# Optimization experiments

Hardware: AMD Instinct MI355X
Metric: run time of the kernel (lower is better)

The kernel has to match this reference:

```python
import jax, jax.numpy as jnp
import numpy as np

NUM_TRUE = 8
NUM_NULL = 2
NUM_EXPERTS = NUM_TRUE + NUM_NULL
TOP_K = 2


def setup_inputs() -> dict:
    key = jax.random.key(0)
    k0, k1, k2 = jax.random.split(key, 3)
    B, S, D = 4, 2048, 1024
    inputs = jax.random.normal(k0, (B, S, D), dtype=jnp.float32)
    gate_w = jax.random.normal(k1, (NUM_EXPERTS, D), dtype=jnp.float32) * 0.02
    gate_b = jnp.zeros((NUM_EXPERTS,), dtype=jnp.float32)
    # expert_w stored as [E, D_in, D_out] so expert i computes x @ expert_w[i] + expert_b[i]
    expert_w = jax.random.normal(k2, (NUM_TRUE, D, D), dtype=jnp.float32) * 0.02
    expert_b = jnp.zeros((NUM_TRUE, D), dtype=jnp.float32)
    return {"inputs": inputs, "gate_w": gate_w, "gate_b": gate_b,
            "expert_w": expert_w, "expert_b": expert_b}


def reference(inputs, gate_w, gate_b, expert_w, expert_b):
    D = inputs.shape[-1]
    x = inputs.reshape(-1, D)                       # [T, D]
    gate_logits = x @ gate_w.T + gate_b             # [T, E]
    gate_probs = jax.nn.softmax(gate_logits, axis=-1)
    weights, selected = jax.lax.top_k(gate_probs, TOP_K)  # [T, K]
    true_mask = selected < NUM_TRUE                 # null experts contribute nothing
    true_weights = weights * true_mask
    denom = true_weights.sum(axis=-1, keepdims=True)
    denom = jnp.where(denom > 0, denom, jnp.ones_like(denom))
    norm_w = (true_weights / denom).astype(x.dtype)  # [T, K]
    # per-(token, true-expert) combine weight; zero for unselected experts
    one_hot = jax.nn.one_hot(selected, NUM_EXPERTS, dtype=norm_w.dtype)  # [T, K, E]
    combine_w = jnp.einsum('tk,tke->te', norm_w, one_hot)[:, :NUM_TRUE]  # [T, E_true]
    # dense expert evaluation, then weighted combine (zero weights cancel
    # exactly as the gather/scatter loop in the torch code)
    expert_out = jnp.einsum('td,edh->teh', x, expert_w) + expert_b[None, :, :]  # [T, E_true, D]
    out = jnp.einsum('te,teh->th', combine_w, expert_out)  # [T, D]
    return out.reshape(inputs.shape[:-1] + (out.shape[-1],))
```

## Files before the change

kernel.cpp:

```cpp
#include <hip/hip_runtime.h>
#include <hip/hip_bf16.h>
#include <stdint.h>

#define T_TOKENS 8192
#define D_DIM    1024
#define NE       10
#define NT       8
#define SEG      2048

typedef unsigned short u16;
typedef __attribute__((ext_vector_type(8))) __bf16 bf16x8;
typedef __attribute__((ext_vector_type(4))) float  f32x4;
typedef __attribute__((ext_vector_type(8))) unsigned short u16x8;
typedef __attribute__((ext_vector_type(4))) unsigned short u16x4;

static __device__ __forceinline__ u16 f32_to_bf16(float f) {
  union { float f; uint32_t u; } v; v.f = f;
  uint32_t u = v.u;
  return (u16)((u + 0x7fffu + ((u >> 16) & 1u)) >> 16);
}
static __device__ __forceinline__ float bf16_to_f32(u16 u) {
  union { uint32_t u; float f; } v; v.u = ((uint32_t)u) << 16; return v.f;
}

static __device__ __forceinline__ void async_load16(const u16* g, u16* l) {
  __builtin_amdgcn_global_load_lds(
      (const __attribute__((address_space(1))) void*)(const void*)g,
      (__attribute__((address_space(3))) void*)(void*)l, 16, 0, 0);
}

union PrepShared {
  struct { float gws[NE * D_DIM]; float gbs[NE]; int se[32]; float swt[32]; } g;
  struct { float tile[64][65]; } t;
};

__global__ __launch_bounds__(256) void prep_kernel(
    const float* __restrict__ x, const float* __restrict__ gw,
    const float* __restrict__ gb, const float* __restrict__ W,
    u16* __restrict__ xb, u16* __restrict__ wT,
    int* __restrict__ cnt, int* __restrict__ tokList,
    int* __restrict__ revIdx, float* __restrict__ revW) {
  __shared__ PrepShared sh;
  int tid = threadIdx.x;

  if (blockIdx.x >= 512) {
    int tb = blockIdx.x - 512;
    int e  = tb >> 8;
    int rem = tb & 255;
    int k0 = (rem >> 4) * 64;
    int n0 = (rem & 15) * 64;
    int c  = tid & 63;
    int r0 = tid >> 6;
    const float* We = W + ((size_t)e << 20);
#pragma unroll
    for (int rr = 0; rr < 16; ++rr) {
      int r = rr * 4 + r0;
      sh.t.tile[c][r] = We[(size_t)(k0 + r) * 1024 + n0 + c];
    }
    __syncthreads();
    u16* wTe = wT + ((size_t)e << 20);
#pragma unroll
    for (int rr = 0; rr < 16; ++rr) {
      int n = rr * 4 + r0;
      wTe[(size_t)(n0 + n) * 1024 + k0 + c] = f32_to_bf16(sh.t.tile[n][c]);
    }
    return;
  }

  {
    const f32x4* g4 = (const f32x4*)gw;
    f32x4* s4 = (f32x4*)sh.g.gws;
    for (int i = tid; i < NE * D_DIM / 4; i += 256) s4[i] = g4[i];
  }
  if (tid < NE) sh.g.gbs[tid] = gb[tid];
  __syncthreads();
  int lane = tid & 63;
  int wv   = tid >> 6;
  const f32x4* gws4 = (const f32x4*)sh.g.gws;
  for (int it = 0; it < 4; ++it) {
    int slot = wv * 4 + it;
    int t = blockIdx.x * 16 + slot;
    const f32x4* xr4 = (const f32x4*)(x + (size_t)t * D_DIM);
    f32x4 xv[4];
#pragma unroll
    for (int jj = 0; jj < 4; ++jj) xv[jj] = xr4[lane + 64 * jj];
    u16x4* xbr = (u16x4*)(xb + (size_t)t * D_DIM);
#pragma unroll
    for (int jj = 0; jj < 4; ++jj) {
      u16x4 pk;
#pragma unroll
      for (int k = 0; k < 4; ++k) pk[k] = f32_to_bf16(xv[jj][k]);
      xbr[lane + 64 * jj] = pk;
    }
    float logit[NE];
#pragma unroll
    for (int e = 0; e < NE; ++e) {
      float a = 0.f;
#pragma unroll
      for (int jj = 0; jj < 4; ++jj) {
        f32x4 gv = gws4[e * 256 + lane + 64 * jj];
#pragma unroll
        for (int k = 0; k < 4; ++k) a = fmaf(xv[jj][k], gv[k], a);
      }
#pragma unroll
      for (int off = 32; off >= 1; off >>= 1) a += __shfl_xor(a, off);
      logit[e] = a + sh.g.gbs[e];
    }
    float mx = logit[0];
#pragma unroll
    for (int e = 1; e < NE; ++e) mx = fmaxf(mx, logit[e]);
    float p[NE]; float s = 0.f;
#pragma unroll
    for (int e = 0; e < NE; ++e) { p[e] = expf(logit[e] - mx); s += p[e]; }
    int e0 = 0; float b0 = p[0];
#pragma unroll
    for (int e = 1; e < NE; ++e) if (p[e] > b0) { b0 = p[e]; e0 = e; }
    int e1 = -1; float b1 = -1.f;
#pragma unroll
    for (int e = 0; e < NE; ++e) if (e != e0 && p[e] > b1) { b1 = p[e]; e1 = e; }
    float w0 = b0 / s, w1 = b1 / s;
    float tw0 = (e0 < NT) ? w0 : 0.f;
    float tw1 = (e1 < NT) ? w1 : 0.f;
    float denom = tw0 + tw1;
    float nw0 = 0.f, nw1 = 0.f;
    if (denom > 0.f) { nw0 = tw0 / denom; nw1 = tw1 / denom; }
    if (lane == 0) {
      sh.g.se[slot * 2]     = (e0 < NT) ? e0 : -1;  sh.g.swt[slot * 2]     = nw0;
      sh.g.se[slot * 2 + 1] = (e1 < NT) ? e1 : -1;  sh.g.swt[slot * 2 + 1] = nw1;
      if (e0 >= NT) { revIdx[t * 2]     = -1; revW[t * 2]     = 0.f; }
      if (e1 >= NT) { revIdx[t * 2 + 1] = -1; revW[t * 2 + 1] = 0.f; }
    }
  }
  __syncthreads();
  if (tid < NT) {
    int e = tid, c = 0;
    for (int i = 0; i < 32; ++i) c += (sh.g.se[i] == e);
    if (c > 0) {
      int base = atomicAdd(&cnt[e * 32], c);
      int j = 0;
      for (int i = 0; i < 32; ++i) {
        if (sh.g.se[i] == e) {
          int tt  = blockIdx.x * 16 + (i >> 1);
          int pos = base + j;
          tokList[e * SEG + pos]   = tt;
          revIdx[tt * 2 + (i & 1)] = e * SEG + pos;
          revW[tt * 2 + (i & 1)]   = sh.g.swt[i];
          ++j;
        }
      }
    }
  }
}

__global__ __launch_bounds__(256) void moe_gemm(
    const u16* __restrict__ xb, const u16* __restrict__ wT,
    const int* __restrict__ cnt, const int* __restrict__ tokList,
    const float* __restrict__ eb, u16* __restrict__ ybuf) {
  int e  = blockIdx.x;
  int c  = cnt[e * 32];
  int m0 = blockIdx.z * 128;
  if (m0 >= c) return;
  int n0 = blockIdx.y * 128;
  __shared__ __align__(16) u16 As[3][128 * 32];
  __shared__ __align__(16) u16 Bs[3][128 * 32];
  __shared__ int tokS[128];
  int tid = threadIdx.x;
  if (tid < 128) {
    int gm = m0 + tid;
    tokS[tid] = (gm < c) ? tokList[e * SEG + gm] : tokList[e * SEG];
  }
  __syncthreads();
  int lane = tid & 63;
  int wv   = tid >> 6;
  int rl  = lane >> 2;
  int kcp = lane & 3;
  int kcd = kcp ^ (rl & 3);
  int rowL0 = wv * 32 + rl, rowL1 = rowL0 + 16;
  const u16* gA0 = xb + (size_t)tokS[rowL0] * 1024 + kcd * 8;
  const u16* gA1 = xb + (size_t)tokS[rowL1] * 1024 + kcd * 8;
  const u16* wTe = wT + ((size_t)e << 20);
  const u16* gB0 = wTe + (size_t)(n0 + rowL0) * 1024 + kcd * 8;
  const u16* gB1 = wTe + (size_t)(n0 + rowL1) * 1024 + kcd * 8;
  int ldsA0 = (wv * 32) * 32, ldsA1 = (wv * 32 + 16) * 32;

  int wm = wv >> 1, wn = wv & 1;
  int lrow = lane & 15;
  int q    = lane >> 4;
  int sw   = (q ^ (lrow & 3)) * 8;
  f32x4 acc[4][4];
#pragma unroll
  for (int i = 0; i < 4; ++i)
#pragma unroll
    for (int j = 0; j < 4; ++j) acc[i][j] = (f32x4){0.f, 0.f, 0.f, 0.f};

#pragma unroll
  for (int p = 0; p < 2; ++p) {
    int ko = p * 32;
    async_load16(gA0 + ko, As[p] + ldsA0);
    async_load16(gA1 + ko, As[p] + ldsA1);
    async_load16(gB0 + ko, Bs[p] + ldsA0);
    async_load16(gB1 + ko, Bs[p] + ldsA1);
  }

  int cur = 0;
  for (int kt = 0; kt < 32; ++kt) {
    asm volatile("s_barrier" ::: "memory");
    if (kt < 30) {
      int st = cur - 1; if (st < 0) st += 3;
      int ko = (kt + 2) * 32;
      async_load16(gA0 + ko, As[st] + ldsA0);
      async_load16(gA1 + ko, As[st] + ldsA1);
      async_load16(gB0 + ko, Bs[st] + ldsA0);
      async_load16(gB1 + ko, Bs[st] + ldsA1);
      asm volatile("s_waitcnt vmcnt(8)" ::: "memory");
    } else if (kt == 30) {
      asm volatile("s_waitcnt vmcnt(4)" ::: "memory");
    } else {
      asm volatile("s_waitcnt vmcnt(0)" ::: "memory");
    }
    asm volatile("s_barrier" ::: "memory");
    bf16x8 af[4], bfr[4];
#pragma unroll
    for (int mt = 0; mt < 4; ++mt)
      af[mt] = *(const bf16x8*)(As[cur] + (wm * 64 + mt * 16 + lrow) * 32 + sw);
#pragma unroll
    for (int nt = 0; nt < 4; ++nt)
      bfr[nt] = *(const bf16x8*)(Bs[cur] + (wn * 64 + nt * 16 + lrow) * 32 + sw);
#pragma unroll
    for (int mt = 0; mt < 4; ++mt)
#pragma unroll
      for (int nt = 0; nt < 4; ++nt)
        acc[mt][nt] = __builtin_amdgcn_mfma_f32_16x16x32_bf16(
            af[mt], bfr[nt], acc[mt][nt], 0, 0, 0);
    ++cur; if (cur == 3) cur = 0;
  }
  int rq = lane >> 4;
  float bias[4];
#pragma unroll
  for (int nt = 0; nt < 4; ++nt)
    bias[nt] = eb[e * 1024 + n0 + wn * 64 + nt * 16 + lrow];
  u16* yb = ybuf + ((size_t)(e * SEG + m0)) * 1024 + n0 + wn * 64 + lrow;
#pragma unroll
  for (int mt = 0; mt < 4; ++mt) {
#pragma unroll
    for (int r = 0; r < 4; ++r) {
      int ml = wm * 64 + mt * 16 + rq * 4 + r;
      u16* row = yb + (size_t)ml * 1024;
#pragma unroll
      for (int nt = 0; nt < 4; ++nt)
        row[nt * 16] = f32_to_bf16(acc[mt][nt][r] + bias[nt]);
    }
  }
}

__global__ __launch_bounds__(256) void combine_kernel(
    const u16* __restrict__ ybuf, const int* __restrict__ revIdx,
    const float* __restrict__ revW, float* __restrict__ out) {
  int tid = threadIdx.x, lane = tid & 63, wv = tid >> 6;
  for (int it = 0; it < 4; ++it) {
    int t  = blockIdx.x * 16 + wv * 4 + it;
    int i0 = revIdx[t * 2], i1 = revIdx[t * 2 + 1];
    float w0 = revW[t * 2], w1 = revW[t * 2 + 1];
    float o[16];
#pragma unroll
    for (int k = 0; k < 16; ++k) o[k] = 0.f;
    if (i0 >= 0) {
      const u16x8* y = (const u16x8*)(ybuf + (size_t)i0 * 1024);
#pragma unroll
      for (int jj = 0; jj < 2; ++jj) {
        u16x8 v = y[lane + 64 * jj];
#pragma unroll
        for (int k = 0; k < 8; ++k) o[jj * 8 + k] += w0 * bf16_to_f32(v[k]);
      }
    }
    if (i1 >= 0) {
      const u16x8* y = (const u16x8*)(ybuf + (size_t)i1 * 1024);
#pragma unroll
      for (int jj = 0; jj < 2; ++jj) {
        u16x8 v = y[lane + 64 * jj];
#pragma unroll
        for (int k = 0; k < 8; ++k) o[jj * 8 + k] += w1 * bf16_to_f32(v[k]);
      }
    }
    f32x4* o4 = (f32x4*)(out + (size_t)t * 1024);
#pragma unroll
    for (int jj = 0; jj < 2; ++jj)
#pragma unroll
      for (int h = 0; h < 2; ++h) {
        f32x4 vv = {o[jj * 8 + h * 4], o[jj * 8 + h * 4 + 1],
                    o[jj * 8 + h * 4 + 2], o[jj * 8 + h * 4 + 3]};
        o4[2 * (lane + 64 * jj) + h] = vv;
      }
  }
}

extern "C" void kernel_launch(void* const* d_in, const int* in_sizes, int n_in,
                              void* d_out, int out_size, void* d_ws, size_t ws_size,
                              hipStream_t stream) {
  const float* x  = (const float*)d_in[0];
  const float* gw = (const float*)d_in[1];
  const float* gb = (const float*)d_in[2];
  const float* ew = (const float*)d_in[3];
  const float* eb = (const float*)d_in[4];
  float* out = (float*)d_out;
  char* ws = (char*)d_ws;
  int*   cnt     = (int*)ws;
  int*   tokList = (int*)(ws + 4096);
  int*   revIdx  = (int*)(ws + 4096 + 65536);
  float* revW    = (float*)(ws + 4096 + 131072);
  u16*   xb      = (u16*)(ws + 200704);
  u16*   wT      = (u16*)(ws + 200704 + 16777216);
  u16*   ybuf    = (u16*)(ws + 200704 + 33554432);

  hipMemsetAsync(cnt, 0, 4096, stream);
  prep_kernel<<<2560, 256, 0, stream>>>(x, gw, gb, ew, xb, wT, cnt, tokList,
                                        revIdx, revW);
  moe_gemm<<<dim3(8, 8, 16), 256, 0, stream>>>(xb, wT, cnt, tokList, eb, ybuf);
  combine_kernel<<<512, 256, 0, stream>>>(ybuf, revIdx, revW, out);
}
```

Before: 177.4 us.

## Replace LDS async staging with direct global-to-register double-buffered loads

The expert GEMM no longer stages A and B tiles through a triple-buffered LDS pipeline with global_load_lds and barriers. Each wave now loads its MFMA fragments straight from global memory into registers, with a two-deep register double buffer. This removes LDS traffic and the block-wide barriers. In exchange, each fragment is fetched redundantly by several waves, and accesses are less coalesced. The final prefetch also reads beyond the last K block.

```diff
diff --git a/kernel.cpp b/kernel.cpp
--- a/kernel.cpp
+++ b/kernel.cpp
@@ -21,12 +21,6 @@
 }
 static __device__ __forceinline__ float bf16_to_f32(u16 u) {
   union { uint32_t u; float f; } v; v.u = ((uint32_t)u) << 16; return v.f;
-}
-
-static __device__ __forceinline__ void async_load16(const u16* g, u16* l) {
-  __builtin_amdgcn_global_load_lds(
-      (const __attribute__((address_space(1))) void*)(const void*)g,
-      (__attribute__((address_space(3))) void*)(void*)l, 16, 0, 0);
 }
 
 union PrepShared {
@@ -161,8 +155,6 @@
   int m0 = blockIdx.z * 128;
   if (m0 >= c) return;
   int n0 = blockIdx.y * 128;
-  __shared__ __align__(16) u16 As[3][128 * 32];
-  __shared__ __align__(16) u16 Bs[3][128 * 32];
   __shared__ int tokS[128];
   int tid = threadIdx.x;
   if (tid < 128) {
@@ -172,67 +164,52 @@
   __syncthreads();
   int lane = tid & 63;
   int wv   = tid >> 6;
-  int rl  = lane >> 2;
-  int kcp = lane & 3;
-  int kcd = kcp ^ (rl & 3);
-  int rowL0 = wv * 32 + rl, rowL1 = rowL0 + 16;
-  const u16* gA0 = xb + (size_t)tokS[rowL0] * 1024 + kcd * 8;
-  const u16* gA1 = xb + (size_t)tokS[rowL1] * 1024 + kcd * 8;
-  const u16* wTe = wT + ((size_t)e << 20);
-  const u16* gB0 = wTe + (size_t)(n0 + rowL0) * 1024 + kcd * 8;
-  const u16* gB1 = wTe + (size_t)(n0 + rowL1) * 1024 + kcd * 8;
-  int ldsA0 = (wv * 32) * 32, ldsA1 = (wv * 32 + 16) * 32;
-
   int wm = wv >> 1, wn = wv & 1;
   int lrow = lane & 15;
   int q    = lane >> 4;
-  int sw   = (q ^ (lrow & 3)) * 8;
+  const u16* wTe = wT + ((size_t)e << 20);
+  int aO[4], bO[4];
+#pragma unroll
+  for (int mt = 0; mt < 4; ++mt)
+    aO[mt] = tokS[wm * 64 + mt * 16 + lrow] * 1024 + q * 8;
+#pragma unroll
+  for (int nt = 0; nt < 4; ++nt)
+    bO[nt] = (n0 + wn * 64 + nt * 16 + lrow) * 1024 + q * 8;
+
   f32x4 acc[4][4];
 #pragma unroll
   for (int i = 0; i < 4; ++i)
 #pragma unroll
     for (int j = 0; j < 4; ++j) acc[i][j] = (f32x4){0.f, 0.f, 0.f, 0.f};
 
-#pragma unroll
-  for (int p = 0; p < 2; ++p) {
-    int ko = p * 32;
-    async_load16(gA0 + ko, As[p] + ldsA0);
-    async_load16(gA1 + ko, As[p] + ldsA1);
-    async_load16(gB0 + ko, Bs[p] + ldsA0);
-    async_load16(gB1 + ko, Bs[p] + ldsA1);
-  }
-
-  int cur = 0;
-  for (int kt = 0; kt < 32; ++kt) {
-    asm volatile("s_barrier" ::: "memory");
-    if (kt < 30) {
-      int st = cur - 1; if (st < 0) st += 3;
-      int ko = (kt + 2) * 32;
-      async_load16(gA0 + ko, As[st] + ldsA0);
-      async_load16(gA1 + ko, As[st] + ldsA1);
-      async_load16(gB0 + ko, Bs[st] + ldsA0);
-      async_load16(gB1 + ko, Bs[st] + ldsA1);
-      asm volatile("s_waitcnt vmcnt(8)" ::: "memory");
-    } else if (kt == 30) {
-      asm volatile("s_waitcnt vmcnt(4)" ::: "memory");
-    } else {
-      asm volatile("s_waitcnt vmcnt(0)" ::: "memory");
-    }
-    asm volatile("s_barrier" ::: "memory");
-    bf16x8 af[4], bfr[4];
-#pragma unroll
-    for (int mt = 0; mt < 4; ++mt)
-      af[mt] = *(const bf16x8*)(As[cur] + (wm * 64 + mt * 16 + lrow) * 32 + sw);
-#pragma unroll
-    for (int nt = 0; nt < 4; ++nt)
-      bfr[nt] = *(const bf16x8*)(Bs[cur] + (wn * 64 + nt * 16 + lrow) * 32 + sw);
+  bf16x8 aC[4], bC[4], aN[4], bN[4];
+#pragma unroll
+  for (int mt = 0; mt < 4; ++mt) aC[mt] = *(const bf16x8*)(xb + aO[mt]);
+#pragma unroll
+  for (int nt = 0; nt < 4; ++nt) bC[nt] = *(const bf16x8*)(wTe + bO[nt]);
+
+#pragma unroll 1
+  for (int kb = 0; kb < 1024; kb += 64) {
+#pragma unroll
+    for (int mt = 0; mt < 4; ++mt) aN[mt] = *(const bf16x8*)(xb + aO[mt] + kb + 32);
+#pragma unroll
+    for (int nt = 0; nt < 4; ++nt) bN[nt] = *(const bf16x8*)(wTe + bO[nt] + kb + 32);
 #pragma unroll
     for (int mt = 0; mt < 4; ++mt)
 #pragma unroll
       for (int nt = 0; nt < 4; ++nt)
         acc[mt][nt] = __builtin_amdgcn_mfma_f32_16x16x32_bf16(
-            af[mt], bfr[nt], acc[mt][nt], 0, 0, 0);
-    ++cur; if (cur == 3) cur = 0;
+            aC[mt], bC[nt], acc[mt][nt], 0, 0, 0);
+#pragma unroll
+    for (int mt = 0; mt < 4; ++mt) aC[mt] = *(const bf16x8*)(xb + aO[mt] + kb + 64);
+#pragma unroll
+    for (int nt = 0; nt < 4; ++nt) bC[nt] = *(const bf16x8*)(wTe + bO[nt] + kb + 64);
+#pragma unroll
+    for (int mt = 0; mt < 4; ++mt)
+#pragma unroll
+      for (int nt = 0; nt < 4; ++nt)
+        acc[mt][nt] = __builtin_amdgcn_mfma_f32_16x16x32_bf16(
+            aN[mt], bN[nt], acc[mt][nt], 0, 0, 0);
   }
   int rq = lane >> 4;
   float bias[4];
```

After: 252.4 us. 1.42x slower.
